# Kernel tuning notes

Measured on AMD Instinct MI355X. Metric: run time of the kernel, lower is better.

The kernel has to match this reference:

```python
import jax, jax.numpy as jnp
import numpy as np

B, D, H = 65536, 3, 256  # collocation batch, coord dim, hidden width


def setup_inputs() -> dict:
    key = jax.random.key(0)
    ks = jax.random.split(key, 8)

    def init(k, shape, fan_in):
        return jax.random.normal(k, shape, dtype=jnp.float32) * np.float32(1.0 / np.sqrt(fan_in))

    return {
        "x": jax.random.uniform(ks[0], (B, D), dtype=jnp.float32, minval=0.1, maxval=1.0),
        "W0": init(ks[1], (D, H), D), "b0": jnp.zeros((H,), jnp.float32),
        "W1": init(ks[2], (H, H), H), "b1": jnp.zeros((H,), jnp.float32),
        "W2": init(ks[3], (H, H), H), "b2": jnp.zeros((H,), jnp.float32),
        "W3": init(ks[4], (H, H), H), "b3": jnp.zeros((H,), jnp.float32),
        "Wout": init(ks[5], (H, 1), H), "bout": jnp.zeros((1,), jnp.float32),
    }


def reference(x, W0, b0, W1, b1, W2, b2, W3, b3, Wout, bout):
    # Scalar PINN network u(xi), xi: [D]
    def u_fn(xi):
        h = jnp.tanh(xi @ W0 + b0)
        h = jnp.tanh(h @ W1 + b1)
        h = jnp.tanh(h @ W2 + b2)
        h = jnp.tanh(h @ W3 + b3)
        return (h @ Wout + bout)[0]

    u = jax.vmap(u_fn)(x)                               # [B]
    # batch_gradient: du/dx_i for every coordinate axis (Cartesian: no adjustment)
    grads = jax.vmap(jax.grad(u_fn))(x)                 # [B, D]
    # batch_hessian diagonal: d^2u/dx_i^2 via forward-over-reverse
    hess_fn = jax.jacfwd(jax.grad(u_fn))                # [D, D] per sample
    hess_diag = jax.vmap(lambda xi: jnp.diagonal(hess_fn(xi)))(x)  # [B, D]
    # pack (u, grad, hessian-diagonal) as the PDE-residual ingredients
    return jnp.concatenate([u[:, None], grads, hess_diag], axis=1)  # [B, 1+D+D]
```

## Files before the change

### kernel.cpp

```cpp
#include <hip/hip_runtime.h>
#include <hip/hip_fp16.h>

#define HDIM 256
#define MS 16
#define LDAK 264
#define CSTRIDE (MS * LDAK * 2)

typedef _Float16 half8 __attribute__((ext_vector_type(8)));
typedef _Float16 half4 __attribute__((ext_vector_type(4)));
typedef _Float16 half2v __attribute__((ext_vector_type(2)));
typedef __fp16  fp16x2 __attribute__((ext_vector_type(2)));
typedef __fp16  fp16x8 __attribute__((ext_vector_type(8)));
typedef float f32x4 __attribute__((ext_vector_type(4)));

__device__ __forceinline__ float fast_tanh(float x) {
    float e = __expf(2.0f * x);
    return 1.0f - 2.0f * __builtin_amdgcn_rcpf(e + 1.0f);
}

__device__ __forceinline__ half4 cvt4(float a, float b, float c, float d) {
    half2v lo = __builtin_bit_cast(half2v, __builtin_amdgcn_cvt_pkrtz(a, b));
    half2v hi = __builtin_bit_cast(half2v, __builtin_amdgcn_cvt_pkrtz(c, d));
    half4 r; r[0] = lo[0]; r[1] = lo[1]; r[2] = hi[0]; r[3] = hi[1];
    return r;
}

__global__ __launch_bounds__(256) void pack_weights(const float* __restrict__ W1,
                                                    const float* __restrict__ W2,
                                                    const float* __restrict__ W3,
                                                    const float* __restrict__ Wout,
                                                    _Float16* __restrict__ out) {
    if (blockIdx.x == 96) {
        int t = threadIdx.x;
        if (t < HDIM) out[3 * 65536 + t] = (_Float16)Wout[t];
        return;
    }
    int tid = blockIdx.x * 256 + threadIdx.x;
    int l = tid >> 13;
    int idx = tid & 8191;
    int kg = idx >> 8;
    int n = idx & 255;
    const float* W = (l == 0) ? W1 : (l == 1) ? W2 : W3;
    half8 v;
    #pragma unroll
    for (int j = 0; j < 8; ++j) v[j] = (_Float16)W[(kg * 8 + j) * 256 + n];
    *(half8*)(out + l * 65536 + kg * 2048 + n * 8) = v;
}

__global__ __launch_bounds__(256, 2)
void pinn_fused(const float* __restrict__ x,
                const float* __restrict__ W0,
                const float* __restrict__ b0,
                const float* __restrict__ b1,
                const float* __restrict__ b2,
                const float* __restrict__ b3,
                const _Float16* __restrict__ Wq,
                const float* __restrict__ bout,
                const _Float16* __restrict__ Wp,
                float* __restrict__ out) {
    __shared__ __align__(16) _Float16 Abuf[7 * MS][LDAK];

    const int tid  = threadIdx.x;
    const int lane = tid & 63;
    const int wid  = tid >> 6;
    const int qd   = lane >> 4;
    const int n15  = lane & 15;
    const int base = blockIdx.x * MS;
    const int nw   = wid * 64 + n15;

    const int voff0 = (qd * 256 + nw) * 8;

    half8 wf[3][4];
    #pragma unroll
    for (int t = 0; t < 4; ++t)
        wf[0][t] = *(const half8*)(Wp + 0 * 8192 + voff0 + t * 128);
    #pragma unroll
    for (int t = 0; t < 4; ++t)
        wf[1][t] = *(const half8*)(Wp + 1 * 8192 + voff0 + t * 128);

    {
        const int m  = tid & 15;
        const int nb = (tid >> 4) * 16;
        const float x0 = x[(base + m) * 3 + 0];
        const float x1 = x[(base + m) * 3 + 1];
        const float x2 = x[(base + m) * 3 + 2];
        #pragma unroll
        for (int ch = 0; ch < 2; ++ch) {
            const int n0 = nb + ch * 8;
            f32x4 w0v[2], w1v[2], w2v[2], bv[2];
            w0v[0] = *(const f32x4*)(W0 + n0);            w0v[1] = *(const f32x4*)(W0 + n0 + 4);
            w1v[0] = *(const f32x4*)(W0 + HDIM + n0);     w1v[1] = *(const f32x4*)(W0 + HDIM + n0 + 4);
            w2v[0] = *(const f32x4*)(W0 + 2 * HDIM + n0); w2v[1] = *(const f32x4*)(W0 + 2 * HDIM + n0 + 4);
            bv[0]  = *(const f32x4*)(b0 + n0);            bv[1]  = *(const f32x4*)(b0 + n0 + 4);
            half8 h[7];
            #pragma unroll
            for (int r = 0; r < 8; ++r) {
                const float w0 = w0v[r >> 2][r & 3];
                const float w1 = w1v[r >> 2][r & 3];
                const float w2 = w2v[r >> 2][r & 3];
                float z  = x0 * w0 + x1 * w1 + x2 * w2 + bv[r >> 2][r & 3];
                float tv = fast_tanh(z);
                float dd = 1.f - tv * tv;
                float c2 = -2.f * tv * dd;
                h[0][r] = (_Float16)tv;
                h[1][r] = (_Float16)(dd * w0);
                h[2][r] = (_Float16)(dd * w1);
                h[3][r] = (_Float16)(dd * w2);
                h[4][r] = (_Float16)(c2 * w0 * w0);
                h[5][r] = (_Float16)(c2 * w1 * w1);
                h[6][r] = (_Float16)(c2 * w2 * w2);
            }
            #pragma unroll
            for (int c = 0; c < 7; ++c)
                *(half8*)&Abuf[c * MS + m][n0] = h[c];
        }
    }
    __syncthreads();

    const char* Ab = (const char*)Abuf;
    const int abase = (n15 * LDAK + qd * 8) * 2;
    char* Sb = (char*)Abuf;
    const int sbase = (n15 * LDAK + wid * 64 + qd * 4) * 2;

    #pragma unroll
    for (int l = 0; l < 3; ++l) {
        const float* bb = (l == 0) ? b1 : (l == 1) ? b2 : b3;

        f32x4 acc[7][4];
        #pragma unroll
        for (int c = 0; c < 7; ++c)
            #pragma unroll
            for (int t = 0; t < 4; ++t) acc[c][t] = (f32x4){0.f, 0.f, 0.f, 0.f};

        #pragma unroll
        for (int s = 0; s < 8; ++s) {
            const int g = l * 8 + s;
            if (g + 2 < 24) {
                #pragma unroll
                for (int t = 0; t < 4; ++t)
                    wf[(g + 2) % 3][t] =
                        *(const half8*)(Wp + (g + 2) * 8192 + voff0 + t * 128);
            }
            half8 af[7];
            #pragma unroll
            for (int c = 0; c < 7; ++c)
                af[c] = *(const half8*)(Ab + abase + c * CSTRIDE + s * 64);
            #pragma unroll
            for (int c = 0; c < 7; ++c)
                #pragma unroll
                for (int t = 0; t < 4; ++t)
                    acc[c][t] = __builtin_amdgcn_mfma_f32_16x16x32_f16(wf[g % 3][t], af[c], acc[c][t], 0, 0, 0);
        }
        __syncthreads();

        #pragma unroll
        for (int t = 0; t < 4; ++t) {
            const int ncol = wid * 64 + t * 16 + qd * 4;
            f32x4 bv = *(const f32x4*)(bb + ncol);
            float tv[4], gj[3][4], sj[3][4];
            #pragma unroll
            for (int r = 0; r < 4; ++r) {
                float zv = acc[0][t][r] + bv[r];
                tv[r] = fast_tanh(zv);
                float dd = 1.f - tv[r] * tv[r];
                float c2 = -2.f * tv[r] * dd;
                #pragma unroll
                for (int i = 0; i < 3; ++i) {
                    float zg = acc[1 + i][t][r];
                    float zs = acc[4 + i][t][r];
                    gj[i][r] = dd * zg;
                    sj[i][r] = dd * zs + c2 * zg * zg;
                }
            }
            *(half4*)(Sb + sbase + 0 * CSTRIDE + t * 32) = cvt4(tv[0], tv[1], tv[2], tv[3]);
            #pragma unroll
            for (int i = 0; i < 3; ++i) {
                *(half4*)(Sb + sbase + (1 + i) * CSTRIDE + t * 32) =
                    cvt4(gj[i][0], gj[i][1], gj[i][2], gj[i][3]);
                *(half4*)(Sb + sbase + (4 + i) * CSTRIDE + t * 32) =
                    cvt4(sj[i][0], sj[i][1], sj[i][2], sj[i][3]);
            }
        }
        __syncthreads();
    }

    if (tid < 7 * MS * 2) {
        const int row = tid >> 1;
        const int h   = tid & 1;
        const _Float16* rp = &Abuf[row][h * 128];
        const _Float16* wq = Wq + h * 128;
        float accv = 0.f;
        #pragma unroll
        for (int kg = 0; kg < 16; ++kg) {
            fp16x8 av = *(const fp16x8*)&rp[kg * 8];
            fp16x8 wv = *(const fp16x8*)&wq[kg * 8];
#if __has_builtin(__builtin_amdgcn_fdot2)
            accv = __builtin_amdgcn_fdot2(__builtin_shufflevector(av, av, 0, 1),
                                          __builtin_shufflevector(wv, wv, 0, 1), accv, false);
            accv = __builtin_amdgcn_fdot2(__builtin_shufflevector(av, av, 2, 3),
                                          __builtin_shufflevector(wv, wv, 2, 3), accv, false);
            accv = __builtin_amdgcn_fdot2(__builtin_shufflevector(av, av, 4, 5),
                                          __builtin_shufflevector(wv, wv, 4, 5), accv, false);
            accv = __builtin_amdgcn_fdot2(__builtin_shufflevector(av, av, 6, 7),
                                          __builtin_shufflevector(wv, wv, 6, 7), accv, false);
#else
            #pragma unroll
            for (int j = 0; j < 8; ++j) accv += (float)av[j] * (float)wv[j];
#endif
        }
        accv += __shfl_xor(accv, 1, 64);
        if (h == 0) {
            const int c = row >> 4;
            const int m = row & 15;
            if (c == 0) accv += bout[0];
            out[(base + m) * 7 + c] = accv;
        }
    }
}

extern "C" void kernel_launch(void* const* d_in, const int* in_sizes, int n_in,
                              void* d_out, int out_size, void* d_ws, size_t ws_size,
                              hipStream_t stream) {
    const float* xp   = (const float*)d_in[0];
    const float* W0   = (const float*)d_in[1];
    const float* b0   = (const float*)d_in[2];
    const float* W1   = (const float*)d_in[3];
    const float* b1   = (const float*)d_in[4];
    const float* W2   = (const float*)d_in[5];
    const float* b2   = (const float*)d_in[6];
    const float* W3   = (const float*)d_in[7];
    const float* b3   = (const float*)d_in[8];
    const float* Wout = (const float*)d_in[9];
    const float* bout = (const float*)d_in[10];
    _Float16* Wp = (_Float16*)d_ws;
    const _Float16* Wq = Wp + 3 * 65536;

    pack_weights<<<97, 256, 0, stream>>>(W1, W2, W3, Wout, Wp);
    pinn_fused<<<65536 / MS, 256, 0, stream>>>(xp, W0, b0, b1, b2, b3, Wq, bout, Wp,
                                               (float*)d_out);
}
```

Before: 255.1 us.

## Ping-pong LDS activation buffers and software-prefetch A fragments across K-steps

Splits the single shared activation buffer into two ping-pong buffers, so each layer reads from one and writes to the other. This removes the barrier between the MFMA loop and the epilogue writes. It also double-buffers the A-fragment LDS loads, prefetching step s+1 while step s's MFMAs run. Shared memory doubles to about 118 KB through dynamic allocation, and launch bounds drop to one block per SIMD group. The extra registers and LDS may lower occupancy, which could cancel the overlap gain.

```diff
diff --git a/kernel.cpp b/kernel.cpp
--- a/kernel.cpp
+++ b/kernel.cpp
@@ -5,11 +5,12 @@
 #define MS 16
 #define LDAK 264
 #define CSTRIDE (MS * LDAK * 2)
+#define ABUF_HALVES (7 * MS * LDAK)
+#define SMEM_BYTES (2 * ABUF_HALVES * 2)
 
 typedef _Float16 half8 __attribute__((ext_vector_type(8)));
 typedef _Float16 half4 __attribute__((ext_vector_type(4)));
 typedef _Float16 half2v __attribute__((ext_vector_type(2)));
-typedef __fp16  fp16x2 __attribute__((ext_vector_type(2)));
 typedef __fp16  fp16x8 __attribute__((ext_vector_type(8)));
 typedef float f32x4 __attribute__((ext_vector_type(4)));
 
@@ -47,7 +48,7 @@
     *(half8*)(out + l * 65536 + kg * 2048 + n * 8) = v;
 }
 
-__global__ __launch_bounds__(256, 2)
+__global__ __launch_bounds__(256, 1)
 void pinn_fused(const float* __restrict__ x,
                 const float* __restrict__ W0,
                 const float* __restrict__ b0,
@@ -58,7 +59,9 @@
                 const float* __restrict__ bout,
                 const _Float16* __restrict__ Wp,
                 float* __restrict__ out) {
-    __shared__ __align__(16) _Float16 Abuf[7 * MS][LDAK];
+    extern __shared__ __align__(16) _Float16 smem[];
+    _Float16* const bufA = smem;
+    _Float16* const bufB = smem + ABUF_HALVES;
 
     const int tid  = threadIdx.x;
     const int lane = tid & 63;
@@ -112,25 +115,30 @@
             }
             #pragma unroll
             for (int c = 0; c < 7; ++c)
-                *(half8*)&Abuf[c * MS + m][n0] = h[c];
+                *(half8*)&bufA[(c * MS + m) * LDAK + n0] = h[c];
         }
     }
     __syncthreads();
 
-    const char* Ab = (const char*)Abuf;
     const int abase = (n15 * LDAK + qd * 8) * 2;
-    char* Sb = (char*)Abuf;
     const int sbase = (n15 * LDAK + wid * 64 + qd * 4) * 2;
 
     #pragma unroll
     for (int l = 0; l < 3; ++l) {
         const float* bb = (l == 0) ? b1 : (l == 1) ? b2 : b3;
+        const char* Ab = (const char*)((l & 1) ? bufB : bufA);
+        char* Sb = (char*)((l & 1) ? bufA : bufB);
 
         f32x4 acc[7][4];
         #pragma unroll
         for (int c = 0; c < 7; ++c)
             #pragma unroll
             for (int t = 0; t < 4; ++t) acc[c][t] = (f32x4){0.f, 0.f, 0.f, 0.f};
+
+        half8 af[2][7];
+        #pragma unroll
+        for (int c = 0; c < 7; ++c)
+            af[0][c] = *(const half8*)(Ab + abase + c * CSTRIDE);
 
         #pragma unroll
         for (int s = 0; s < 8; ++s) {
@@ -141,17 +149,18 @@
                     wf[(g + 2) % 3][t] =
                         *(const half8*)(Wp + (g + 2) * 8192 + voff0 + t * 128);
             }
-            half8 af[7];
+            if (s < 7) {
+                #pragma unroll
+                for (int c = 0; c < 7; ++c)
+                    af[(s + 1) & 1][c] =
+                        *(const half8*)(Ab + abase + c * CSTRIDE + (s + 1) * 64);
+            }
             #pragma unroll
             for (int c = 0; c < 7; ++c)
-                af[c] = *(const half8*)(Ab + abase + c * CSTRIDE + s * 64);
-            #pragma unroll
-            for (int c = 0; c < 7; ++c)
                 #pragma unroll
                 for (int t = 0; t < 4; ++t)
-                    acc[c][t] = __builtin_amdgcn_mfma_f32_16x16x32_f16(wf[g % 3][t], af[c], acc[c][t], 0, 0, 0);
-        }
-        __syncthreads();
+                    acc[c][t] = __builtin_amdgcn_mfma_f32_16x16x32_f16(wf[g % 3][t], af[s & 1][c], acc[c][t], 0, 0, 0);
+        }
 
         #pragma unroll
         for (int t = 0; t < 4; ++t) {
@@ -187,7 +196,7 @@
     if (tid < 7 * MS * 2) {
         const int row = tid >> 1;
         const int h   = tid & 1;
-        const _Float16* rp = &Abuf[row][h * 128];
+        const _Float16* rp = &bufB[row * LDAK + h * 128];
         const _Float16* wq = Wq + h * 128;
         float accv = 0.f;
         #pragma unroll
@@ -235,7 +244,11 @@
     _Float16* Wp = (_Float16*)d_ws;
     const _Float16* Wq = Wp + 3 * 65536;
 
+    hipFuncSetAttribute((const void*)pinn_fused,
+                        hipFuncAttributeMaxDynamicSharedMemorySize, SMEM_BYTES);
+
     pack_weights<<<97, 256, 0, stream>>>(W1, W2, W3, Wout, Wp);
-    pinn_fused<<<65536 / MS, 256, 0, stream>>>(xp, W0, b0, b1, b2, b3, Wq, bout, Wp,
-                                               (float*)d_out);
-}
+    pinn_fused<<<65536 / MS, 256, SMEM_BYTES, stream>>>(xp, W0, b0, b1, b2, b3,
+                                                        Wq, bout, Wp,
+                                                        (float*)d_out);
+}
```

Result: slower. 295.5 us (+15.8%).

## Fuse output projection into last layer epilogue and use lightweight LDS barriers

Applied to the files above, without the earlier changes.

The final hidden layer no longer writes its fp16 tanh/gradient/hessian activations back to LDS for a separate dot-product pass against Wout. Instead each lane multiplies its fp32 activations by Wout in registers, reduces across quads with shuffles, and sums four per-wave partials through a small shared buffer. This removes one LDS round trip, a barrier and the fp16 rounding of the last layer. __syncthreads is also replaced by an inline-asm s_waitcnt lgkmcnt(0) plus s_barrier, which skips waiting on outstanding global loads such as the prefetched weights.

```diff
diff --git a/kernel.cpp b/kernel.cpp
--- a/kernel.cpp
+++ b/kernel.cpp
@@ -9,8 +9,6 @@
 typedef _Float16 half8 __attribute__((ext_vector_type(8)));
 typedef _Float16 half4 __attribute__((ext_vector_type(4)));
 typedef _Float16 half2v __attribute__((ext_vector_type(2)));
-typedef __fp16  fp16x2 __attribute__((ext_vector_type(2)));
-typedef __fp16  fp16x8 __attribute__((ext_vector_type(8)));
 typedef float f32x4 __attribute__((ext_vector_type(4)));
 
 __device__ __forceinline__ float fast_tanh(float x) {
@@ -25,16 +23,14 @@
     return r;
 }
 
+__device__ __forceinline__ void barrier_lds() {
+    asm volatile("s_waitcnt lgkmcnt(0)\n\ts_barrier" ::: "memory");
+}
+
 __global__ __launch_bounds__(256) void pack_weights(const float* __restrict__ W1,
                                                     const float* __restrict__ W2,
                                                     const float* __restrict__ W3,
-                                                    const float* __restrict__ Wout,
                                                     _Float16* __restrict__ out) {
-    if (blockIdx.x == 96) {
-        int t = threadIdx.x;
-        if (t < HDIM) out[3 * 65536 + t] = (_Float16)Wout[t];
-        return;
-    }
     int tid = blockIdx.x * 256 + threadIdx.x;
     int l = tid >> 13;
     int idx = tid & 8191;
@@ -54,11 +50,12 @@
                 const float* __restrict__ b1,
                 const float* __restrict__ b2,
                 const float* __restrict__ b3,
-                const _Float16* __restrict__ Wq,
+                const float* __restrict__ Wout,
                 const float* __restrict__ bout,
                 const _Float16* __restrict__ Wp,
                 float* __restrict__ out) {
     __shared__ __align__(16) _Float16 Abuf[7 * MS][LDAK];
+    __shared__ float part[4 * 7 * MS];
 
     const int tid  = threadIdx.x;
     const int lane = tid & 63;
@@ -115,7 +112,7 @@
                 *(half8*)&Abuf[c * MS + m][n0] = h[c];
         }
     }
-    __syncthreads();
+    barrier_lds();
 
     const char* Ab = (const char*)Abuf;
     const int abase = (n15 * LDAK + qd * 8) * 2;
@@ -123,8 +120,8 @@
     const int sbase = (n15 * LDAK + wid * 64 + qd * 4) * 2;
 
     #pragma unroll
-    for (int l = 0; l < 3; ++l) {
-        const float* bb = (l == 0) ? b1 : (l == 1) ? b2 : b3;
+    for (int l = 0; l < 2; ++l) {
+        const float* bb = (l == 0) ? b1 : b2;
 
         f32x4 acc[7][4];
         #pragma unroll
@@ -135,7 +132,7 @@
         #pragma unroll
         for (int s = 0; s < 8; ++s) {
             const int g = l * 8 + s;
-            if (g + 2 < 24) {
+            {
                 #pragma unroll
                 for (int t = 0; t < 4; ++t)
                     wf[(g + 2) % 3][t] =
@@ -151,7 +148,7 @@
                 for (int t = 0; t < 4; ++t)
                     acc[c][t] = __builtin_amdgcn_mfma_f32_16x16x32_f16(wf[g % 3][t], af[c], acc[c][t], 0, 0, 0);
         }
-        __syncthreads();
+        barrier_lds();
 
         #pragma unroll
         for (int t = 0; t < 4; ++t) {
@@ -181,40 +178,78 @@
                     cvt4(sj[i][0], sj[i][1], sj[i][2], sj[i][3]);
             }
         }
-        __syncthreads();
-    }
-
-    if (tid < 7 * MS * 2) {
-        const int row = tid >> 1;
-        const int h   = tid & 1;
-        const _Float16* rp = &Abuf[row][h * 128];
-        const _Float16* wq = Wq + h * 128;
-        float accv = 0.f;
-        #pragma unroll
-        for (int kg = 0; kg < 16; ++kg) {
-            fp16x8 av = *(const fp16x8*)&rp[kg * 8];
-            fp16x8 wv = *(const fp16x8*)&wq[kg * 8];
-#if __has_builtin(__builtin_amdgcn_fdot2)
-            accv = __builtin_amdgcn_fdot2(__builtin_shufflevector(av, av, 0, 1),
-                                          __builtin_shufflevector(wv, wv, 0, 1), accv, false);
-            accv = __builtin_amdgcn_fdot2(__builtin_shufflevector(av, av, 2, 3),
-                                          __builtin_shufflevector(wv, wv, 2, 3), accv, false);
-            accv = __builtin_amdgcn_fdot2(__builtin_shufflevector(av, av, 4, 5),
-                                          __builtin_shufflevector(wv, wv, 4, 5), accv, false);
-            accv = __builtin_amdgcn_fdot2(__builtin_shufflevector(av, av, 6, 7),
-                                          __builtin_shufflevector(wv, wv, 6, 7), accv, false);
-#else
-            #pragma unroll
-            for (int j = 0; j < 8; ++j) accv += (float)av[j] * (float)wv[j];
-#endif
-        }
-        accv += __shfl_xor(accv, 1, 64);
-        if (h == 0) {
-            const int c = row >> 4;
-            const int m = row & 15;
-            if (c == 0) accv += bout[0];
-            out[(base + m) * 7 + c] = accv;
-        }
+        barrier_lds();
+    }
+
+    {
+        f32x4 acc[7][4];
+        #pragma unroll
+        for (int c = 0; c < 7; ++c)
+            #pragma unroll
+            for (int t = 0; t < 4; ++t) acc[c][t] = (f32x4){0.f, 0.f, 0.f, 0.f};
+
+        #pragma unroll
+        for (int s = 0; s < 8; ++s) {
+            const int g = 16 + s;
+            if (g + 2 < 24) {
+                #pragma unroll
+                for (int t = 0; t < 4; ++t)
+                    wf[(g + 2) % 3][t] =
+                        *(const half8*)(Wp + (g + 2) * 8192 + voff0 + t * 128);
+            }
+            half8 af[7];
+            #pragma unroll
+            for (int c = 0; c < 7; ++c)
+                af[c] = *(const half8*)(Ab + abase + c * CSTRIDE + s * 64);
+            #pragma unroll
+            for (int c = 0; c < 7; ++c)
+                #pragma unroll
+                for (int t = 0; t < 4; ++t)
+                    acc[c][t] = __builtin_amdgcn_mfma_f32_16x16x32_f16(wf[g % 3][t], af[c], acc[c][t], 0, 0, 0);
+        }
+
+        float p[7] = {0.f, 0.f, 0.f, 0.f, 0.f, 0.f, 0.f};
+        #pragma unroll
+        for (int t = 0; t < 4; ++t) {
+            const int ncol = wid * 64 + t * 16 + qd * 4;
+            f32x4 bv = *(const f32x4*)(b3 + ncol);
+            f32x4 wv = *(const f32x4*)(Wout + ncol);
+            #pragma unroll
+            for (int r = 0; r < 4; ++r) {
+                float zv = acc[0][t][r] + bv[r];
+                float tv = fast_tanh(zv);
+                float dd = 1.f - tv * tv;
+                float c2 = -2.f * tv * dd;
+                p[0] += tv * wv[r];
+                #pragma unroll
+                for (int i = 0; i < 3; ++i) {
+                    float zg = acc[1 + i][t][r];
+                    float zs = acc[4 + i][t][r];
+                    p[1 + i] += (dd * zg) * wv[r];
+                    p[4 + i] += (dd * zs + c2 * zg * zg) * wv[r];
+                }
+            }
+        }
+        #pragma unroll
+        for (int c = 0; c < 7; ++c) {
+            p[c] += __shfl_xor(p[c], 16, 64);
+            p[c] += __shfl_xor(p[c], 32, 64);
+        }
+        if (lane < 16) {
+            #pragma unroll
+            for (int c = 0; c < 7; ++c)
+                part[(wid * 7 + c) * MS + lane] = p[c];
+        }
+    }
+    barrier_lds();
+
+    if (tid < 7 * MS) {
+        const int c = tid >> 4;
+        const int m = tid & 15;
+        float v = part[(0 * 7 + c) * MS + m] + part[(1 * 7 + c) * MS + m] +
+                  part[(2 * 7 + c) * MS + m] + part[(3 * 7 + c) * MS + m];
+        if (c == 0) v += bout[0];
+        out[(base + m) * 7 + c] = v;
     }
 }
 
@@ -233,9 +268,8 @@
     const float* Wout = (const float*)d_in[9];
     const float* bout = (const float*)d_in[10];
     _Float16* Wp = (_Float16*)d_ws;
-    const _Float16* Wq = Wp + 3 * 65536;
-
-    pack_weights<<<97, 256, 0, stream>>>(W1, W2, W3, Wout, Wp);
-    pinn_fused<<<65536 / MS, 256, 0, stream>>>(xp, W0, b0, b1, b2, b3, Wq, bout, Wp,
+
+    pack_weights<<<96, 256, 0, stream>>>(W1, W2, W3, Wp);
+    pinn_fused<<<65536 / MS, 256, 0, stream>>>(xp, W0, b0, b1, b2, b3, Wout, bout, Wp,
                                                (float*)d_out);
 }
```

Result: faster. 244.0 us (-4.3%).
